# Kernel tuning notes

Measured on AMD Instinct MI355X. Metric: run time of the kernel, lower is better.

## Reference

```python
import jax, jax.numpy as jnp
import numpy as np

EMB, HEADS = 1024, 16

def setup_inputs() -> dict:
    key = jax.random.key(0)
    ks = jax.random.split(key, 6)
    B, T, C = 2, 2048, EMB
    s = 0.02
    return {
        "x": jax.random.normal(ks[0], (B, T, C), dtype=jnp.float32),
        "Wq": jax.random.normal(ks[1], (C, C), dtype=jnp.float32) * s,
        "Wk": jax.random.normal(ks[2], (C, C), dtype=jnp.float32) * s,
        "Wv": jax.random.normal(ks[3], (C, C), dtype=jnp.float32) * s,
        "Wo": jax.random.normal(ks[4], (C, C), dtype=jnp.float32) * s,
        "bo": jnp.zeros((C,), dtype=jnp.float32),
    }

def reference(x, Wq, Wk, Wv, Wo, bo):
    B, T, C = x.shape
    H = HEADS
    S = C // H
    # torch nn.Linear: y = x @ W.T
    q = (x @ Wq.T).reshape(B, T, H, S)
    k = (x @ Wk.T).reshape(B, T, H, S)
    v = (x @ Wv.T).reshape(B, T, H, S)
    # scores [B,H,T,T]
    dot = jnp.einsum("bthd,bshd->bhts", q, k) / jnp.sqrt(jnp.float32(S))
    causal = jnp.tril(jnp.ones((T, T), dtype=bool))  # keep lower triangle
    dot = jnp.where(causal, dot, -jnp.inf)
    attn = jax.nn.softmax(dot, axis=-1)  # dropout is identity (eval / p=0)
    out = jnp.einsum("bhts,bshd->bthd", attn, v).reshape(B, T, C)
    return out @ Wo.T + bo
```

## Files before the change

kernel.cpp:

```cpp
#include <hip/hip_runtime.h>

#define BB 2
#define TT 2048
#define CC 1024
#define HH 16
#define SS 64
#define MM (BB * TT)

typedef unsigned short u16;
typedef __bf16 bf16x8 __attribute__((ext_vector_type(8)));
typedef float f32x4 __attribute__((ext_vector_type(4)));
typedef float f32x16 __attribute__((ext_vector_type(16)));

#define MFMA16(a, b, c) __builtin_amdgcn_mfma_f32_16x16x32_bf16((a), (b), (c), 0, 0, 0)
#define MFMA32(a, b, c) __builtin_amdgcn_mfma_f32_32x32x16_bf16((a), (b), (c), 0, 0, 0)
#define CVTPK(d, a, b) asm("v_cvt_pk_bf16_f32 %0, %1, %2" : "=v"(d) : "v"(a), "v"(b))

__device__ inline u16 f2bf(float f) {
    union { float f; unsigned u; } v;
    v.f = f;
    unsigned r = v.u + 0x7FFFu + ((v.u >> 16) & 1u);
    return (u16)(r >> 16);
}

__global__ __launch_bounds__(256) void cast_all(
    const float4* __restrict__ x,  const float4* __restrict__ wq,
    const float4* __restrict__ wk, const float4* __restrict__ wv,
    const float4* __restrict__ wo,
    ushort4* __restrict__ xo, ushort4* __restrict__ qo,
    ushort4* __restrict__ ko, ushort4* __restrict__ vo,
    ushort4* __restrict__ oo) {
    int bid = blockIdx.x;
    const float4* src; ushort4* dst; int i;
    if (bid < 4096) {
        src = x; dst = xo; i = bid * 256 + threadIdx.x;
    } else {
        int s = (bid - 4096) >> 10;
        int r = (bid - 4096) & 1023;
        src = (s == 0) ? wq : (s == 1) ? wk : (s == 2) ? wv : wo;
        dst = (s == 0) ? qo : (s == 1) ? ko : (s == 2) ? vo : oo;
        i = r * 256 + threadIdx.x;
    }
    float4 v = src[i];
    ushort4 o;
    o.x = f2bf(v.x); o.y = f2bf(v.y); o.z = f2bf(v.z); o.w = f2bf(v.w);
    dst[i] = o;
}

__device__ __forceinline__ void stage_tile64(const u16* __restrict__ g, int row0,
                                             int k0, u16* lds) {
    int t = threadIdx.x;
#pragma unroll
    for (int q = 0; q < 4; ++q) {
        int idx = q * 256 + t;
        int row = idx >> 3;
        int col = idx & 7;
        int scol = col ^ (row & 7);
        const u16* src = g + (long)(row0 + row) * CC + k0 + scol * 8;
        __builtin_amdgcn_global_load_lds(
            (const __attribute__((address_space(1))) void*)src,
            (__attribute__((address_space(3))) void*)(lds + idx * 8), 16, 0, 0);
    }
}

__device__ __forceinline__ void gemm_core(const u16* __restrict__ A,
                                          const u16* __restrict__ Bt,
                                          int blkM, int blkN,
                                          u16* sm,
                                          f32x4 (&acc)[4][4]) {
    int lane = threadIdx.x & 63;
    int w = threadIdx.x >> 6;
    int wr = w >> 1, wc = w & 1;
    int l15 = lane & 15;
    int hi = lane >> 4;
    const int NT = CC / 64;

    u16* bufA = sm;
    u16* bufB = sm + 16384;

#pragma unroll
    for (int m = 0; m < 4; ++m)
#pragma unroll
        for (int n = 0; n < 4; ++n) acc[m][n] = (f32x4){0.f, 0.f, 0.f, 0.f};

    stage_tile64(A, blkM * 128, 0, bufA);
    stage_tile64(Bt, blkN * 128, 0, bufB);
    stage_tile64(A, blkM * 128, 64, bufA + 8192);
    stage_tile64(Bt, blkN * 128, 64, bufB + 8192);

    for (int kt = 0; kt < NT; ++kt) {
        if (kt + 1 < NT) {
            asm volatile("s_waitcnt vmcnt(8)" ::: "memory");
        } else {
            asm volatile("s_waitcnt vmcnt(0)" ::: "memory");
        }
        __builtin_amdgcn_s_barrier();
        __builtin_amdgcn_sched_barrier(0);

        u16* cA = bufA + (kt & 1) * 8192;
        u16* cB = bufB + (kt & 1) * 8192;

#pragma unroll
        for (int half = 0; half < 2; ++half) {
            bf16x8 af[4], bfr[4];
#pragma unroll
            for (int m = 0; m < 4; ++m) {
                int row = wr * 64 + m * 16 + l15;
                int ch = (half * 4 + hi) ^ (row & 7);
                af[m] = *(const bf16x8*)(cA + row * 64 + ch * 8);
            }
#pragma unroll
            for (int n = 0; n < 4; ++n) {
                int row = wc * 64 + n * 16 + l15;
                int ch = (half * 4 + hi) ^ (row & 7);
                bfr[n] = *(const bf16x8*)(cB + row * 64 + ch * 8);
            }
#pragma unroll
            for (int m = 0; m < 4; ++m)
#pragma unroll
                for (int n = 0; n < 4; ++n)
                    acc[m][n] = MFMA16(af[m], bfr[n], acc[m][n]);
        }

        __builtin_amdgcn_s_barrier();
        if (kt + 2 < NT) {
            stage_tile64(A, blkM * 128, (kt + 2) * 64, bufA + (kt & 1) * 8192);
            stage_tile64(Bt, blkN * 128, (kt + 2) * 64, bufB + (kt & 1) * 8192);
        }
    }
}

__global__ __launch_bounds__(256) void qkv_gemm(const u16* __restrict__ xb,
                                                const u16* __restrict__ wqb,
                                                const u16* __restrict__ wkb,
                                                const u16* __restrict__ wvb,
                                                u16* __restrict__ qo,
                                                u16* __restrict__ kpk,
                                                u16* __restrict__ vpk) {
    __shared__ u16 smem[8 * 128 * 32];
    int seg = blockIdx.x >> 8;
    int bid = blockIdx.x & 255;
    int blkM = bid & 31, blkN = bid >> 5;
    const u16* Bt = (seg == 0) ? wqb : (seg == 1) ? wkb : wvb;
    f32x4 acc[4][4];
    gemm_core(xb, Bt, blkM, blkN, smem, acc);

    int lane = threadIdx.x & 63;
    int w = threadIdx.x >> 6, wr = w >> 1, wc = w & 1;
    int l15 = lane & 15, hi = lane >> 4;
    int r0 = blkM * 128 + wr * 64 + hi * 4;
    int c0 = blkN * 128 + wc * 64 + l15;

    if (seg == 0) {
        const float sc = 0.18033688011112042f;
#pragma unroll
        for (int m = 0; m < 4; ++m)
#pragma unroll
            for (int n = 0; n < 4; ++n)
#pragma unroll
                for (int i = 0; i < 4; ++i)
                    qo[(long)(r0 + m * 16 + i) * CC + c0 + n * 16] =
                        f2bf(acc[m][n][i] * sc);
        return;
    }

    u16* sl = smem;
    __syncthreads();

    int ltb = wr * 64 + hi * 4;
    int lfb = wc * 64;
    if (seg == 1) {
#pragma unroll
        for (int m = 0; m < 4; ++m) {
            int lt = ltb + m * 16;
            int kvbl = lt >> 5;
#pragma unroll
            for (int n = 0; n < 4; ++n) {
                int lf = lfb + n * 16 + l15;
                int dd = lf & 63, hhl = lf >> 6;
                int base = ((kvbl << 1) + hhl) * 2048 + ((dd >> 3) << 8) + (dd & 7);
#pragma unroll
                for (int i = 0; i < 4; ++i)
                    sl[base + ((lt + i) & 31) * 8] = f2bf(acc[m][n][i]);
            }
        }
    } else {
#pragma unroll
        for (int m = 0; m < 4; ++m) {
            int lt = ltb + m * 16;
            int kvbl = lt >> 5, kv0 = lt & 31;
#pragma unroll
            for (int n = 0; n < 4; ++n) {
                int lf = lfb + n * 16 + l15;
                int dd = lf & 63, hhl = lf >> 6;
                int off = ((kvbl << 1) + hhl) * 2048 +
                          ((((dd >> 5) << 2) + (kv0 >> 3)) << 8) +
                          ((dd & 31) << 3) + (kv0 & 7);
                ushort4 p;
                p.x = f2bf(acc[m][n][0]); p.y = f2bf(acc[m][n][1]);
                p.z = f2bf(acc[m][n][2]); p.w = f2bf(acc[m][n][3]);
                *(ushort4*)(sl + off) = p;
            }
        }
    }
    __syncthreads();

    u16* pk = (seg == 1) ? kpk : vpk;
    int t = threadIdx.x;
    int b2 = blkM >> 4;
    int kvb_base = (blkM * 4) & 63;
#pragma unroll
    for (int q = 0; q < 8; ++q) {
        int kvbl = q >> 1, hhl = q & 1;
        long g = (((long)(b2 * 16 + blkN * 2 + hhl) * 64) + kvb_base + kvbl) << 11;
        bf16x8 v = *(const bf16x8*)(sl + q * 2048 + t * 8);
        *(bf16x8*)(pk + g + t * 8) = v;
    }
}

__global__ __launch_bounds__(256) void out_gemm(const u16* __restrict__ at,
                                                const u16* __restrict__ wob,
                                                const float* __restrict__ bias,
                                                float* __restrict__ out) {
    __shared__ u16 smem[8 * 128 * 32];
    int bid = blockIdx.x;
    int blkM = bid & 31, blkN = bid >> 5;
    f32x4 acc[4][4];
    gemm_core(at, wob, blkM, blkN, smem, acc);

    int lane = threadIdx.x & 63;
    int w = threadIdx.x >> 6, wr = w >> 1, wc = w & 1;
    int l15 = lane & 15, hi = lane >> 4;
    int r0 = blkM * 128 + wr * 64 + hi * 4;
    int c0 = blkN * 128 + wc * 64 + l15;
#pragma unroll
    for (int n = 0; n < 4; ++n) {
        int c = c0 + n * 16;
        float bv = bias[c];
#pragma unroll
        for (int m = 0; m < 4; ++m)
#pragma unroll
            for (int i = 0; i < 4; ++i)
                out[(long)(r0 + m * 16 + i) * CC + c] = acc[m][n][i] + bv;
    }
}

__global__ __launch_bounds__(128, 4) void attn_fwd(const u16* __restrict__ Q,
                                                   const u16* __restrict__ Kp,
                                                   const u16* __restrict__ Vp,
                                                   u16* __restrict__ O) {
    __shared__ float xch[64 * 36];
    int lane = threadIdx.x & 63;
    int w = threadIdx.x >> 6;
    int bh = blockIdx.x & 31;
    int qt = 63 - (blockIdx.x >> 5);
    int h = bh & 15, b = bh >> 4;
    int l31 = lane & 31, h5 = lane >> 5;

    int qg = qt * 32 + l31;
    int nt32 = qt + 1;

    const u16* kbase = Kp + (((long)(b * 16 + h) * 64) << 11) + h5 * 256 + l31 * 8;
    const u16* vbase = Vp + (((long)(b * 16 + h) * 64) << 11) + h5 * 256 + l31 * 8;

    const u16* qrow = Q + (long)(b * TT + qg) * CC + h * SS + h5 * 8;
    bf16x8 qf[4];
#pragma unroll
    for (int m = 0; m < 4; ++m) qf[m] = *(const bf16x8*)(qrow + m * 16);

    f32x16 oa0 = {0.f}, oa1 = {0.f};
    f32x16 ls = {0.f};

#pragma unroll 1
    for (int tt = w; tt < nt32; tt += 2) {
        const u16* kt = kbase + ((long)tt << 11);
        const u16* vt2 = vbase + ((long)tt << 11);

        bf16x8 kf0 = *(const bf16x8*)(kt);
        bf16x8 kf1 = *(const bf16x8*)(kt + 512);
        bf16x8 kf2 = *(const bf16x8*)(kt + 1024);
        bf16x8 kf3 = *(const bf16x8*)(kt + 1536);
        bf16x8 v00 = *(const bf16x8*)(vt2);
        bf16x8 v01 = *(const bf16x8*)(vt2 + 512);
        bf16x8 v10 = *(const bf16x8*)(vt2 + 1024);
        bf16x8 v11 = *(const bf16x8*)(vt2 + 1536);

        f32x16 s0 = {0.f};
        __builtin_amdgcn_s_setprio(1);
        s0 = MFMA32(kf0, qf[0], s0);
        s0 = MFMA32(kf1, qf[1], s0);
        s0 = MFMA32(kf2, qf[2], s0);
        s0 = MFMA32(kf3, qf[3], s0);
        __builtin_amdgcn_s_setprio(0);

        if (tt == qt) {
            int kvb = tt * 32 + 4 * h5;
#pragma unroll
            for (int r = 0; r < 16; ++r) {
                int kv = kvb + (r & 3) + 8 * (r >> 2);
                if (kv > qg) s0[r] = -1e30f;
            }
        }

        f32x16 p0v;
#pragma unroll
        for (int r = 0; r < 16; ++r) p0v[r] = __builtin_amdgcn_exp2f(s0[r] - 16.0f);
#pragma unroll
        for (int r = 0; r < 16; ++r) ls[r] += p0v[r];

        bf16x8 pf[2];
#pragma unroll
        for (int hk = 0; hk < 2; ++hk) {
            unsigned w0, w1, w2, w3;
            CVTPK(w0, p0v[8 * hk + 0], p0v[8 * hk + 1]);
            CVTPK(w1, p0v[8 * hk + 2], p0v[8 * hk + 3]);
            CVTPK(w2, p0v[8 * hk + 4], p0v[8 * hk + 5]);
            CVTPK(w3, p0v[8 * hk + 6], p0v[8 * hk + 7]);
            asm("v_permlane32_swap_b32 %0, %1" : "+v"(w0), "+v"(w2));
            asm("v_permlane32_swap_b32 %0, %1" : "+v"(w1), "+v"(w3));
            union { unsigned u[4]; bf16x8 v; } fb;
            fb.u[0] = w0; fb.u[1] = w1; fb.u[2] = w2; fb.u[3] = w3;
            pf[hk] = fb.v;
        }

        __builtin_amdgcn_s_setprio(1);
        oa0 = MFMA32(v00, pf[0], oa0);
        oa0 = MFMA32(v01, pf[1], oa0);
        oa1 = MFMA32(v10, pf[0], oa1);
        oa1 = MFMA32(v11, pf[1], oa1);
        __builtin_amdgcn_s_setprio(0);
    }

    float l;
    {
        float t8[8];
#pragma unroll
        for (int r = 0; r < 8; ++r) t8[r] = ls[r] + ls[r + 8];
#pragma unroll
        for (int r = 0; r < 4; ++r) t8[r] = t8[r] + t8[r + 4];
        l = (t8[0] + t8[1]) + (t8[2] + t8[3]);
        l += __shfl_xor(l, 32);
    }

    if (w == 1) {
        float* xl = xch + lane * 36;
#pragma unroll
        for (int r = 0; r < 16; ++r) { xl[r] = oa0[r]; xl[16 + r] = oa1[r]; }
        xl[32] = l;
    }
    __syncthreads();
    if (w == 0) {
        float* xl = xch + lane * 36;
        float inv = 1.0f / (l + xl[32]);

        u16* ob = O + (long)(b * TT + qg) * CC + h * SS;
#pragma unroll
        for (int rq = 0; rq < 4; ++rq) {
            float v00 = (oa0[rq * 4 + 0] + xl[rq * 4 + 0]) * inv;
            float v01 = (oa0[rq * 4 + 1] + xl[rq * 4 + 1]) * inv;
            float v02 = (oa0[rq * 4 + 2] + xl[rq * 4 + 2]) * inv;
            float v03 = (oa0[rq * 4 + 3] + xl[rq * 4 + 3]) * inv;
            float v10 = (oa1[rq * 4 + 0] + xl[16 + rq * 4 + 0]) * inv;
            float v11 = (oa1[rq * 4 + 1] + xl[16 + rq * 4 + 1]) * inv;
            float v12 = (oa1[rq * 4 + 2] + xl[16 + rq * 4 + 2]) * inv;
            float v13 = (oa1[rq * 4 + 3] + xl[16 + rq * 4 + 3]) * inv;
            unsigned a0, a1, c0, c1;
            CVTPK(a0, v00, v01);
            CVTPK(a1, v02, v03);
            CVTPK(c0, v10, v11);
            CVTPK(c1, v12, v13);
            uint2 ua, uc;
            ua.x = a0; ua.y = a1; uc.x = c0; uc.y = c1;
            *(uint2*)(ob + rq * 8 + h5 * 4) = ua;
            *(uint2*)(ob + 32 + rq * 8 + h5 * 4) = uc;
        }
    }
}

extern "C" void kernel_launch(void* const* d_in, const int* in_sizes, int n_in,
                              void* d_out, int out_size, void* d_ws, size_t ws_size,
                              hipStream_t stream) {
    const float* x  = (const float*)d_in[0];
    const float* Wq = (const float*)d_in[1];
    const float* Wk = (const float*)d_in[2];
    const float* Wv = (const float*)d_in[3];
    const float* Wo = (const float*)d_in[4];
    const float* bo = (const float*)d_in[5];

    char* ws = (char*)d_ws;
    const size_t MB = 1024 * 1024;
    u16* x_bf  = (u16*)(ws);
    u16* wq_bf = (u16*)(ws + 8 * MB);
    u16* wk_bf = (u16*)(ws + 10 * MB);
    u16* wv_bf = (u16*)(ws + 12 * MB);
    u16* wo_bf = (u16*)(ws + 14 * MB);
    u16* q_bf  = (u16*)(ws + 16 * MB);
    u16* kpack = (u16*)(ws + 24 * MB);
    u16* vpack = (u16*)(ws + 32 * MB);
    u16* at_bf = (u16*)(ws + 40 * MB);

    cast_all<<<dim3(8192), dim3(256), 0, stream>>>(
        (const float4*)x, (const float4*)Wq, (const float4*)Wk,
        (const float4*)Wv, (const float4*)Wo,
        (ushort4*)x_bf, (ushort4*)wq_bf, (ushort4*)wk_bf,
        (ushort4*)wv_bf, (ushort4*)wo_bf);

    qkv_gemm<<<dim3(768), dim3(256), 0, stream>>>(x_bf, wq_bf, wk_bf, wv_bf,
                                                  q_bf, kpack, vpack);

    attn_fwd<<<dim3(2048), dim3(128), 0, stream>>>(q_bf, kpack, vpack, at_bf);

    out_gemm<<<dim3(256), dim3(256), 0, stream>>>(at_bf, wo_bf, bo, (float*)d_out);
}
```

Baseline: 82.35 us.

## Process two 32-row query tiles per attention block to reuse K/V loads

```diff
diff --git a/kernel.cpp b/kernel.cpp
--- a/kernel.cpp
+++ b/kernel.cpp
@@ -245,31 +245,37 @@
     }
 }
 
-__global__ __launch_bounds__(128, 4) void attn_fwd(const u16* __restrict__ Q,
+__global__ __launch_bounds__(128, 2) void attn_fwd(const u16* __restrict__ Q,
                                                    const u16* __restrict__ Kp,
                                                    const u16* __restrict__ Vp,
                                                    u16* __restrict__ O) {
-    __shared__ float xch[64 * 36];
+    __shared__ float xch[64 * 68];
     int lane = threadIdx.x & 63;
     int w = threadIdx.x >> 6;
     int bh = blockIdx.x & 31;
-    int qt = 63 - (blockIdx.x >> 5);
+    int qt = 31 - (blockIdx.x >> 5);
     int h = bh & 15, b = bh >> 4;
     int l31 = lane & 31, h5 = lane >> 5;
 
-    int qg = qt * 32 + l31;
-    int nt32 = qt + 1;
+    int qgl = qt * 64 + l31;
+    int qgh = qgl + 32;
+    int nt32 = 2 * qt + 2;
 
     const u16* kbase = Kp + (((long)(b * 16 + h) * 64) << 11) + h5 * 256 + l31 * 8;
     const u16* vbase = Vp + (((long)(b * 16 + h) * 64) << 11) + h5 * 256 + l31 * 8;
 
-    const u16* qrow = Q + (long)(b * TT + qg) * CC + h * SS + h5 * 8;
-    bf16x8 qf[4];
-#pragma unroll
-    for (int m = 0; m < 4; ++m) qf[m] = *(const bf16x8*)(qrow + m * 16);
-
-    f32x16 oa0 = {0.f}, oa1 = {0.f};
-    f32x16 ls = {0.f};
+    const u16* qrl = Q + (long)(b * TT + qgl) * CC + h * SS + h5 * 8;
+    const u16* qrh = Q + (long)(b * TT + qgh) * CC + h * SS + h5 * 8;
+    bf16x8 qfl[4], qfh[4];
+#pragma unroll
+    for (int m = 0; m < 4; ++m) {
+        qfl[m] = *(const bf16x8*)(qrl + m * 16);
+        qfh[m] = *(const bf16x8*)(qrh + m * 16);
+    }
+
+    f32x16 oal0 = {0.f}, oal1 = {0.f};
+    f32x16 oah0 = {0.f}, oah1 = {0.f};
+    f32x16 lsl = {0.f}, lsh = {0.f};
 
 #pragma unroll 1
     for (int tt = w; tt < nt32; tt += 2) {
@@ -285,94 +291,164 @@
         bf16x8 v10 = *(const bf16x8*)(vt2 + 1024);
         bf16x8 v11 = *(const bf16x8*)(vt2 + 1536);
 
-        f32x16 s0 = {0.f};
-        __builtin_amdgcn_s_setprio(1);
-        s0 = MFMA32(kf0, qf[0], s0);
-        s0 = MFMA32(kf1, qf[1], s0);
-        s0 = MFMA32(kf2, qf[2], s0);
-        s0 = MFMA32(kf3, qf[3], s0);
-        __builtin_amdgcn_s_setprio(0);
-
-        if (tt == qt) {
-            int kvb = tt * 32 + 4 * h5;
-#pragma unroll
-            for (int r = 0; r < 16; ++r) {
-                int kv = kvb + (r & 3) + 8 * (r >> 2);
-                if (kv > qg) s0[r] = -1e30f;
-            }
-        }
-
-        f32x16 p0v;
-#pragma unroll
-        for (int r = 0; r < 16; ++r) p0v[r] = __builtin_amdgcn_exp2f(s0[r] - 16.0f);
-#pragma unroll
-        for (int r = 0; r < 16; ++r) ls[r] += p0v[r];
-
-        bf16x8 pf[2];
-#pragma unroll
-        for (int hk = 0; hk < 2; ++hk) {
-            unsigned w0, w1, w2, w3;
-            CVTPK(w0, p0v[8 * hk + 0], p0v[8 * hk + 1]);
-            CVTPK(w1, p0v[8 * hk + 2], p0v[8 * hk + 3]);
-            CVTPK(w2, p0v[8 * hk + 4], p0v[8 * hk + 5]);
-            CVTPK(w3, p0v[8 * hk + 6], p0v[8 * hk + 7]);
-            asm("v_permlane32_swap_b32 %0, %1" : "+v"(w0), "+v"(w2));
-            asm("v_permlane32_swap_b32 %0, %1" : "+v"(w1), "+v"(w3));
-            union { unsigned u[4]; bf16x8 v; } fb;
-            fb.u[0] = w0; fb.u[1] = w1; fb.u[2] = w2; fb.u[3] = w3;
-            pf[hk] = fb.v;
-        }
-
-        __builtin_amdgcn_s_setprio(1);
-        oa0 = MFMA32(v00, pf[0], oa0);
-        oa0 = MFMA32(v01, pf[1], oa0);
-        oa1 = MFMA32(v10, pf[0], oa1);
-        oa1 = MFMA32(v11, pf[1], oa1);
-        __builtin_amdgcn_s_setprio(0);
-    }
-
-    float l;
+        int kvb = tt * 32 + 4 * h5;
+
+        {
+            f32x16 s0 = {0.f};
+            __builtin_amdgcn_s_setprio(1);
+            s0 = MFMA32(kf0, qfl[0], s0);
+            s0 = MFMA32(kf1, qfl[1], s0);
+            s0 = MFMA32(kf2, qfl[2], s0);
+            s0 = MFMA32(kf3, qfl[3], s0);
+            __builtin_amdgcn_s_setprio(0);
+
+            if (tt >= 2 * qt) {
+#pragma unroll
+                for (int r = 0; r < 16; ++r) {
+                    int kv = kvb + (r & 3) + 8 * (r >> 2);
+                    if (kv > qgl) s0[r] = -1e30f;
+                }
+            }
+
+            f32x16 p0v;
+#pragma unroll
+            for (int r = 0; r < 16; ++r)
+                p0v[r] = __builtin_amdgcn_exp2f(s0[r] - 16.0f);
+#pragma unroll
+            for (int r = 0; r < 16; ++r) lsl[r] += p0v[r];
+
+            bf16x8 pf[2];
+#pragma unroll
+            for (int hk = 0; hk < 2; ++hk) {
+                unsigned w0, w1, w2, w3;
+                CVTPK(w0, p0v[8 * hk + 0], p0v[8 * hk + 1]);
+                CVTPK(w1, p0v[8 * hk + 2], p0v[8 * hk + 3]);
+                CVTPK(w2, p0v[8 * hk + 4], p0v[8 * hk + 5]);
+                CVTPK(w3, p0v[8 * hk + 6], p0v[8 * hk + 7]);
+                asm("v_permlane32_swap_b32 %0, %1" : "+v"(w0), "+v"(w2));
+                asm("v_permlane32_swap_b32 %0, %1" : "+v"(w1), "+v"(w3));
+                union { unsigned u[4]; bf16x8 v; } fb;
+                fb.u[0] = w0; fb.u[1] = w1; fb.u[2] = w2; fb.u[3] = w3;
+                pf[hk] = fb.v;
+            }
+
+            __builtin_amdgcn_s_setprio(1);
+            oal0 = MFMA32(v00, pf[0], oal0);
+            oal0 = MFMA32(v01, pf[1], oal0);
+            oal1 = MFMA32(v10, pf[0], oal1);
+            oal1 = MFMA32(v11, pf[1], oal1);
+            __builtin_amdgcn_s_setprio(0);
+        }
+
+        {
+            f32x16 s0 = {0.f};
+            __builtin_amdgcn_s_setprio(1);
+            s0 = MFMA32(kf0, qfh[0], s0);
+            s0 = MFMA32(kf1, qfh[1], s0);
+            s0 = MFMA32(kf2, qfh[2], s0);
+            s0 = MFMA32(kf3, qfh[3], s0);
+            __builtin_amdgcn_s_setprio(0);
+
+            if (tt == 2 * qt + 1) {
+#pragma unroll
+                for (int r = 0; r < 16; ++r) {
+                    int kv = kvb + (r & 3) + 8 * (r >> 2);
+                    if (kv > qgh) s0[r] = -1e30f;
+                }
+            }
+
+            f32x16 p0v;
+#pragma unroll
+            for (int r = 0; r < 16; ++r)
+                p0v[r] = __builtin_amdgcn_exp2f(s0[r] - 16.0f);
+#pragma unroll
+            for (int r = 0; r < 16; ++r) lsh[r] += p0v[r];
+
+            bf16x8 pf[2];
+#pragma unroll
+            for (int hk = 0; hk < 2; ++hk) {
+                unsigned w0, w1, w2, w3;
+                CVTPK(w0, p0v[8 * hk + 0], p0v[8 * hk + 1]);
+                CVTPK(w1, p0v[8 * hk + 2], p0v[8 * hk + 3]);
+                CVTPK(w2, p0v[8 * hk + 4], p0v[8 * hk + 5]);
+                CVTPK(w3, p0v[8 * hk + 6], p0v[8 * hk + 7]);
+                asm("v_permlane32_swap_b32 %0, %1" : "+v"(w0), "+v"(w2));
+                asm("v_permlane32_swap_b32 %0, %1" : "+v"(w1), "+v"(w3));
+                union { unsigned u[4]; bf16x8 v; } fb;
+                fb.u[0] = w0; fb.u[1] = w1; fb.u[2] = w2; fb.u[3] = w3;
+                pf[hk] = fb.v;
+            }
+
+            __builtin_amdgcn_s_setprio(1);
+            oah0 = MFMA32(v00, pf[0], oah0);
+            oah0 = MFMA32(v01, pf[1], oah0);
+            oah1 = MFMA32(v10, pf[0], oah1);
+            oah1 = MFMA32(v11, pf[1], oah1);
+            __builtin_amdgcn_s_setprio(0);
+        }
+    }
+
+    float llo, lhi;
     {
         float t8[8];
 #pragma unroll
-        for (int r = 0; r < 8; ++r) t8[r] = ls[r] + ls[r + 8];
+        for (int r = 0; r < 8; ++r) t8[r] = lsl[r] + lsl[r + 8];
 #pragma unroll
         for (int r = 0; r < 4; ++r) t8[r] = t8[r] + t8[r + 4];
-        l = (t8[0] + t8[1]) + (t8[2] + t8[3]);
-        l += __shfl_xor(l, 32);
+        llo = (t8[0] + t8[1]) + (t8[2] + t8[3]);
+        llo += __shfl_xor(llo, 32);
+#pragma unroll
+        for (int r = 0; r < 8; ++r) t8[r] = lsh[r] + lsh[r + 8];
+#pragma unroll
+        for (int r = 0; r < 4; ++r) t8[r] = t8[r] + t8[r + 4];
+        lhi = (t8[0] + t8[1]) + (t8[2] + t8[3]);
+        lhi += __shfl_xor(lhi, 32);
     }
 
     if (w == 1) {
-        float* xl = xch + lane * 36;
-#pragma unroll
-        for (int r = 0; r < 16; ++r) { xl[r] = oa0[r]; xl[16 + r] = oa1[r]; }
-        xl[32] = l;
+        float* xl = xch + lane * 68;
+#pragma unroll
+        for (int r = 0; r < 16; ++r) {
+            xl[r] = oal0[r];      xl[16 + r] = oal1[r];
+            xl[32 + r] = oah0[r]; xl[48 + r] = oah1[r];
+        }
+        xl[64] = llo; xl[65] = lhi;
     }
     __syncthreads();
     if (w == 0) {
-        float* xl = xch + lane * 36;
-        float inv = 1.0f / (l + xl[32]);
-
-        u16* ob = O + (long)(b * TT + qg) * CC + h * SS;
+        float* xl = xch + lane * 68;
+        float invl = 1.0f / (llo + xl[64]);
+        float invh = 1.0f / (lhi + xl[65]);
+
+        u16* obl = O + (long)(b * TT + qgl) * CC + h * SS;
+        u16* obh = O + (long)(b * TT + qgh) * CC + h * SS;
 #pragma unroll
         for (int rq = 0; rq < 4; ++rq) {
-            float v00 = (oa0[rq * 4 + 0] + xl[rq * 4 + 0]) * inv;
-            float v01 = (oa0[rq * 4 + 1] + xl[rq * 4 + 1]) * inv;
-            float v02 = (oa0[rq * 4 + 2] + xl[rq * 4 + 2]) * inv;
-            float v03 = (oa0[rq * 4 + 3] + xl[rq * 4 + 3]) * inv;
-            float v10 = (oa1[rq * 4 + 0] + xl[16 + rq * 4 + 0]) * inv;
-            float v11 = (oa1[rq * 4 + 1] + xl[16 + rq * 4 + 1]) * inv;
-            float v12 = (oa1[rq * 4 + 2] + xl[16 + rq * 4 + 2]) * inv;
-            float v13 = (oa1[rq * 4 + 3] + xl[16 + rq * 4 + 3]) * inv;
             unsigned a0, a1, c0, c1;
-            CVTPK(a0, v00, v01);
-            CVTPK(a1, v02, v03);
-            CVTPK(c0, v10, v11);
-            CVTPK(c1, v12, v13);
+            CVTPK(a0, (oal0[rq * 4 + 0] + xl[rq * 4 + 0]) * invl,
+                      (oal0[rq * 4 + 1] + xl[rq * 4 + 1]) * invl);
+            CVTPK(a1, (oal0[rq * 4 + 2] + xl[rq * 4 + 2]) * invl,
+                      (oal0[rq * 4 + 3] + xl[rq * 4 + 3]) * invl);
+            CVTPK(c0, (oal1[rq * 4 + 0] + xl[16 + rq * 4 + 0]) * invl,
+                      (oal1[rq * 4 + 1] + xl[16 + rq * 4 + 1]) * invl);
+            CVTPK(c1, (oal1[rq * 4 + 2] + xl[16 + rq * 4 + 2]) * invl,
+                      (oal1[rq * 4 + 3] + xl[16 + rq * 4 + 3]) * invl);
             uint2 ua, uc;
             ua.x = a0; ua.y = a1; uc.x = c0; uc.y = c1;
-            *(uint2*)(ob + rq * 8 + h5 * 4) = ua;
-            *(uint2*)(ob + 32 + rq * 8 + h5 * 4) = uc;
+            *(uint2*)(obl + rq * 8 + h5 * 4) = ua;
+            *(uint2*)(obl + 32 + rq * 8 + h5 * 4) = uc;
+
+            CVTPK(a0, (oah0[rq * 4 + 0] + xl[32 + rq * 4 + 0]) * invh,
+                      (oah0[rq * 4 + 1] + xl[32 + rq * 4 + 1]) * invh);
+            CVTPK(a1, (oah0[rq * 4 + 2] + xl[32 + rq * 4 + 2]) * invh,
+                      (oah0[rq * 4 + 3] + xl[32 + rq * 4 + 3]) * invh);
+            CVTPK(c0, (oah1[rq * 4 + 0] + xl[48 + rq * 4 + 0]) * invh,
+                      (oah1[rq * 4 + 1] + xl[48 + rq * 4 + 1]) * invh);
+            CVTPK(c1, (oah1[rq * 4 + 2] + xl[48 + rq * 4 + 2]) * invh,
+                      (oah1[rq * 4 + 3] + xl[48 + rq * 4 + 3]) * invh);
+            ua.x = a0; ua.y = a1; uc.x = c0; uc.y = c1;
+            *(uint2*)(obh + rq * 8 + h5 * 4) = ua;
+            *(uint2*)(obh + 32 + rq * 8 + h5 * 4) = uc;
         }
     }
 }
@@ -408,7 +484,7 @@
     qkv_gemm<<<dim3(768), dim3(256), 0, stream>>>(x_bf, wq_bf, wk_bf, wv_bf,
                                                   q_bf, kpack, vpack);
 
-    attn_fwd<<<dim3(2048), dim3(128), 0, stream>>>(q_bf, kpack, vpack, at_bf);
+    attn_fwd<<<dim3(1024), dim3(128), 0, stream>>>(q_bf, kpack, vpack, at_bf);
 
     out_gemm<<<dim3(256), dim3(256), 0, stream>>>(at_bf, wo_bf, bo, (float*)d_out);
 }
```

Measured after the change: 85.40 us. 1.04x slower.
